# Performance work log

Hardware: AMD Instinct MI355X
Metric: run time of the kernel (lower is better)

Reference implementation:

```python
import jax, jax.numpy as jnp
import numpy as np

EMBED_DIM = 1024
NUM_HEADS = 16
HEAD_DIM = EMBED_DIM // NUM_HEADS
B, QL, KVL = 2, 2048, 2048


def setup_inputs() -> dict:
    key = jax.random.key(0)
    ks = jax.random.split(key, 16)
    std = 0.02
    inp = {
        "query": jax.random.normal(ks[0], (B, QL, EMBED_DIM), jnp.float32),
        "key": jax.random.normal(ks[1], (B, KVL, EMBED_DIM), jnp.float32),
        "value": jax.random.normal(ks[2], (B, KVL, EMBED_DIM), jnp.float32),
        "logit_scale": jax.random.uniform(ks[3], (1,), jnp.float32),
        "logit_bias": jax.random.normal(ks[4], (1,), jnp.float32),
        "Wq": jax.random.normal(ks[5], (EMBED_DIM, EMBED_DIM), jnp.float32) * std,
        "bq": jnp.zeros((EMBED_DIM,), jnp.float32),
        "Wk": jax.random.normal(ks[6], (EMBED_DIM, EMBED_DIM), jnp.float32) * std,
        "bk": jnp.zeros((EMBED_DIM,), jnp.float32),
        "Wv": jax.random.normal(ks[7], (EMBED_DIM, EMBED_DIM), jnp.float32) * std,
        "bv": jnp.zeros((EMBED_DIM,), jnp.float32),
        "Wo": jax.random.normal(ks[8], (EMBED_DIM, EMBED_DIM), jnp.float32) * std,
        "bo": jnp.zeros((EMBED_DIM,), jnp.float32),
    }
    return inp


def reference(query, key, value, logit_scale, logit_bias, Wq, bq, Wk, bk, Wv, bv, Wo, bo):
    # projections (torch Linear: x @ W.T + b)
    q = query @ Wq.T + bq    # [B, QL, D]
    k = key @ Wk.T + bk      # [B, KVL, D]
    v = value @ Wv.T + bv    # [B, KVL, D]

    # QK L2-normalization over the FULL embed_dim (before head split), per source
    q = q / jnp.linalg.norm(q, axis=-1, keepdims=True)
    k = k / jnp.linalg.norm(k, axis=-1, keepdims=True)
    scale = jnp.exp(logit_scale)  # [1], broadcasts
    bias = logit_bias             # [1], broadcasts

    # split heads: [B, H, L, Dh]
    qh = q.reshape(B, QL, NUM_HEADS, HEAD_DIM).transpose(0, 2, 1, 3)
    kh = k.reshape(B, KVL, NUM_HEADS, HEAD_DIM).transpose(0, 2, 1, 3)
    vh = v.reshape(B, KVL, NUM_HEADS, HEAD_DIM).transpose(0, 2, 1, 3)

    scores = jnp.einsum("bhqd,bhkd->bhqk", qh, kh) * scale + bias  # [B,H,QL,KVL]
    attn = jax.nn.softmax(scores.astype(jnp.float32), axis=-1).astype(qh.dtype)
    # dropout p=0.0 -> identity
    out = jnp.einsum("bhqk,bhkd->bhqd", attn, vh)  # [B,H,QL,Dh]
    out = out.transpose(0, 2, 1, 3).reshape(B, QL, EMBED_DIM)
    out = out @ Wo.T + bo
    return out, attn
```

## Files before the change

kernel.cpp:

```cpp
#include <hip/hip_runtime.h>

#define B_   2
#define L_   2048
#define D_   1024
#define H_   16
#define DH_  64
#define M_TOT (B_ * L_)

typedef __attribute__((ext_vector_type(8))) __bf16 bf16x8;
typedef __attribute__((ext_vector_type(4))) float f32x4;
typedef __attribute__((ext_vector_type(8))) unsigned short u16x8;

__device__ __forceinline__ unsigned short f2bf(float f) {
    unsigned int u = __float_as_uint(f);
    u += 0x7fffu + ((u >> 16) & 1u);
    return (unsigned short)(u >> 16);
}
__device__ __forceinline__ float bf2f(unsigned short u) {
    return __uint_as_float(((unsigned int)u) << 16);
}

__device__ __forceinline__ void gload_lds16(const void* g, void* l) {
    __builtin_amdgcn_global_load_lds(
        (__attribute__((address_space(1))) void*)(void*)g,
        (__attribute__((address_space(3))) void*)l, 16, 0, 0);
}

__global__ __launch_bounds__(256) void cast_in(const float* __restrict__ src,
                                               u16x8* __restrict__ dst)
{
    const int i = blockIdx.x * 256 + threadIdx.x;
    const float4* s = (const float4*)src;
    float4 a = s[2 * i], b = s[2 * i + 1];
    u16x8 w;
    w[0] = f2bf(a.x); w[1] = f2bf(a.y); w[2] = f2bf(a.z); w[3] = f2bf(a.w);
    w[4] = f2bf(b.x); w[5] = f2bf(b.y); w[6] = f2bf(b.z); w[7] = f2bf(b.w);
    dst[i] = w;
}

__global__ __launch_bounds__(256) void cast_w4(const float* __restrict__ Wq,
                                               const float* __restrict__ Wk,
                                               const float* __restrict__ Wv,
                                               const float* __restrict__ Wo,
                                               u16x8* __restrict__ dst)
{
    const int y = blockIdx.y;
    const float* src = (y == 0) ? Wq : (y == 1) ? Wk : (y == 2) ? Wv : Wo;
    const int i = blockIdx.x * 256 + threadIdx.x;
    const float4* s = (const float4*)src;
    float4 a = s[2 * i], b = s[2 * i + 1];
    u16x8 w;
    w[0] = f2bf(a.x); w[1] = f2bf(a.y); w[2] = f2bf(a.z); w[3] = f2bf(a.w);
    w[4] = f2bf(b.x); w[5] = f2bf(b.y); w[6] = f2bf(b.z); w[7] = f2bf(b.w);
    dst[(size_t)y * (D_ * D_ / 8) + i] = w;
}

template<bool F32OUT>
__global__ __launch_bounds__(256) void gemm_nt_mfma(
    const unsigned short* __restrict__ A, const unsigned short* __restrict__ W,
    const float* __restrict__ bias, void* __restrict__ Cout, int K, int N)
{
    __shared__ __align__(16) unsigned short As[128 * 64];
    __shared__ __align__(16) unsigned short Bs[128 * 64];
    const int tid  = threadIdx.x;
    const int bm   = blockIdx.x * 128;
    const int bn   = blockIdx.y * 128;
    const int lane = tid & 63, wid = tid >> 6;
    const int wm   = (wid >> 1) * 64, wn = (wid & 1) * 64;
    const int kg   = lane >> 4, lr = lane & 15;
    const int swz  = lr & 7;

    f32x4 zero = {0.f, 0.f, 0.f, 0.f};
    f32x4 acc[4][4];
    #pragma unroll
    for (int m = 0; m < 4; ++m)
        #pragma unroll
        for (int n = 0; n < 4; ++n) acc[m][n] = zero;

    for (int k0 = 0; k0 < K; k0 += 64) {
        __syncthreads();
        #pragma unroll
        for (int i = 0; i < 4; ++i) {
            int c   = i * 256 + tid;
            int row = c >> 3;
            int c8  = (c & 7) ^ (row & 7);
            gload_lds16(A + (size_t)(bm + row) * K + k0 + c8 * 8, (char*)As + c * 16);
            gload_lds16(W + (size_t)(bn + row) * K + k0 + c8 * 8, (char*)Bs + c * 16);
        }
        __syncthreads();
        #pragma unroll
        for (int ks = 0; ks < 2; ++ks) {
            bf16x8 af[4], bfr[4];
            #pragma unroll
            for (int m = 0; m < 4; ++m)
                af[m] = *(const bf16x8*)((const char*)As +
                        (wm + m * 16 + lr) * 128 + (((ks * 4 + kg) ^ swz) << 4));
            #pragma unroll
            for (int n = 0; n < 4; ++n)
                bfr[n] = *(const bf16x8*)((const char*)Bs +
                        (wn + n * 16 + lr) * 128 + (((ks * 4 + kg) ^ swz) << 4));
            #pragma unroll
            for (int m = 0; m < 4; ++m)
                #pragma unroll
                for (int n = 0; n < 4; ++n)
                    acc[m][n] = __builtin_amdgcn_mfma_f32_16x16x32_bf16(
                        af[m], bfr[n], acc[m][n], 0, 0, 0);
        }
    }

    #pragma unroll
    for (int n = 0; n < 4; ++n) {
        const int col = bn + wn + n * 16 + lr;
        const float bv = bias[col];
        #pragma unroll
        for (int m = 0; m < 4; ++m) {
            const int row0 = bm + wm + m * 16 + kg * 4;
            #pragma unroll
            for (int r = 0; r < 4; ++r) {
                float val = acc[m][n][r] + bv;
                if (F32OUT)
                    ((float*)Cout)[(size_t)(row0 + r) * N + col] = val;
                else
                    ((unsigned short*)Cout)[(size_t)(row0 + r) * N + col] = f2bf(val);
            }
        }
    }
}

__global__ __launch_bounds__(256) void attn_sums(
    const unsigned short* __restrict__ qn, const unsigned short* __restrict__ kn,
    const float* __restrict__ ls, const float* __restrict__ lb,
    float* __restrict__ sums)
{
    __shared__ __align__(16) unsigned short Qs[128 * 64];
    __shared__ __align__(16) unsigned short Ks[128 * 64];
    __shared__ float red[2][128];
    const int z = blockIdx.y, b = z >> 4, h = z & 15;
    const unsigned short* Qp = qn + (size_t)b * L_ * D_ + h * DH_;
    const unsigned short* Kp = kn + (size_t)b * L_ * D_ + h * DH_;

    const int tid  = threadIdx.x;
    const int bm   = blockIdx.x * 128;
    const int lane = tid & 63, wid = tid >> 6;
    const int wq   = wid >> 1, wkv = wid & 1;
    const int kg   = lane >> 4, lr = lane & 15;
    const int swz  = lr & 7;

    #pragma unroll
    for (int i = 0; i < 4; ++i) {
        int c = i * 256 + tid, row = c >> 3, c8 = (c & 7) ^ (row & 7);
        gload_lds16(Qp + (size_t)(bm + row) * D_ + c8 * 8, (char*)Qs + c * 16);
    }

    const float scale = expf(ls[0]);
    const float sb = lb[0];
    f32x4 zero = {0.f, 0.f, 0.f, 0.f};
    float rs[4][4] = {};

    for (int kv0 = 0; kv0 < L_; kv0 += 128) {
        __syncthreads();
        #pragma unroll
        for (int i = 0; i < 4; ++i) {
            int c = i * 256 + tid, row = c >> 3, c8 = (c & 7) ^ (row & 7);
            gload_lds16(Kp + (size_t)(kv0 + row) * D_ + c8 * 8, (char*)Ks + c * 16);
        }
        __syncthreads();
        f32x4 s[4][4];
        #pragma unroll
        for (int m = 0; m < 4; ++m)
            #pragma unroll
            for (int n = 0; n < 4; ++n) s[m][n] = zero;
        #pragma unroll
        for (int ks = 0; ks < 2; ++ks) {
            bf16x8 af[4], bfr[4];
            #pragma unroll
            for (int m = 0; m < 4; ++m)
                af[m] = *(const bf16x8*)((const char*)Qs +
                        (wq * 64 + m * 16 + lr) * 128 + (((ks * 4 + kg) ^ swz) << 4));
            #pragma unroll
            for (int n = 0; n < 4; ++n)
                bfr[n] = *(const bf16x8*)((const char*)Ks +
                        (wkv * 64 + n * 16 + lr) * 128 + (((ks * 4 + kg) ^ swz) << 4));
            #pragma unroll
            for (int m = 0; m < 4; ++m)
                #pragma unroll
                for (int n = 0; n < 4; ++n)
                    s[m][n] = __builtin_amdgcn_mfma_f32_16x16x32_bf16(
                        af[m], bfr[n], s[m][n], 0, 0, 0);
        }
        #pragma unroll
        for (int m = 0; m < 4; ++m)
            #pragma unroll
            for (int n = 0; n < 4; ++n)
                #pragma unroll
                for (int r = 0; r < 4; ++r)
                    rs[m][r] += __expf(s[m][n][r] * scale + sb);
    }

    #pragma unroll
    for (int m = 0; m < 4; ++m)
        #pragma unroll
        for (int r = 0; r < 4; ++r) {
            float sv = rs[m][r];
            sv += __shfl_xor(sv, 1); sv += __shfl_xor(sv, 2);
            sv += __shfl_xor(sv, 4); sv += __shfl_xor(sv, 8);
            if (lr == 0) red[wkv][wq * 64 + m * 16 + kg * 4 + r] = sv;
        }
    __syncthreads();
    if (tid < 128)
        sums[(size_t)z * L_ + bm + tid] = red[0][tid] + red[1][tid];
}

__global__ __launch_bounds__(256) void attn_fused(
    const unsigned short* __restrict__ qn, const unsigned short* __restrict__ kn,
    const unsigned short* __restrict__ Vt, const float* __restrict__ sums,
    const float* __restrict__ ls, const float* __restrict__ lb,
    float* __restrict__ attn, unsigned short* __restrict__ ctx)
{
    __shared__ __align__(16) unsigned short Qs[64 * 64];
    __shared__ __align__(16) unsigned short Ks[128 * 64];
    __shared__ __align__(16) unsigned short Vs[64 * 128];
    __shared__ __align__(16) unsigned short Ps[64 * 128];
    __shared__ float invs[64];
    const int z = blockIdx.y, b = z >> 4, h = z & 15;
    const unsigned short* Qp = qn + (size_t)b * L_ * D_ + h * DH_;
    const unsigned short* Kp = kn + (size_t)b * L_ * D_ + h * DH_;
    const unsigned short* Vp = Vt + (size_t)z * DH_ * L_;
    float* Cp = attn + (size_t)z * L_ * L_;
    unsigned short* Op = ctx + (size_t)b * L_ * D_ + h * DH_;

    const int tid  = threadIdx.x;
    const int bm   = blockIdx.x * 64;
    const int lane = tid & 63, wid = tid >> 6;
    const int wq   = wid >> 1, wkv = wid & 1;
    const int kg   = lane >> 4, lr = lane & 15;
    const int swz  = lr & 7;

    #pragma unroll
    for (int i = 0; i < 2; ++i) {
        int c = i * 256 + tid, row = c >> 3, c8 = (c & 7) ^ (row & 7);
        gload_lds16(Qp + (size_t)(bm + row) * D_ + c8 * 8, (char*)Qs + c * 16);
    }
    if (tid < 64) invs[tid] = 1.0f / sums[(size_t)z * L_ + bm + tid];

    const float scale = expf(ls[0]);
    const float sb = lb[0];
    f32x4 zero = {0.f, 0.f, 0.f, 0.f};
    f32x4 cacc[2][2];
    #pragma unroll
    for (int m = 0; m < 2; ++m) { cacc[m][0] = zero; cacc[m][1] = zero; }

    for (int kv0 = 0; kv0 < L_; kv0 += 128) {
        __syncthreads();
        #pragma unroll
        for (int i = 0; i < 4; ++i) {
            int c = i * 256 + tid, row = c >> 3, c8 = (c & 7) ^ (row & 7);
            gload_lds16(Kp + (size_t)(kv0 + row) * D_ + c8 * 8, (char*)Ks + c * 16);
        }
        #pragma unroll
        for (int i = 0; i < 4; ++i) {
            int c = i * 256 + tid, row = c >> 4, cc = c & 15;
            int sc = cc ^ (row & 7);
            gload_lds16(Vp + (size_t)row * L_ + kv0 + sc * 8, (char*)Vs + c * 16);
        }
        __syncthreads();

        f32x4 s[2][4];
        #pragma unroll
        for (int m = 0; m < 2; ++m)
            #pragma unroll
            for (int n = 0; n < 4; ++n) s[m][n] = zero;
        #pragma unroll
        for (int ks = 0; ks < 2; ++ks) {
            bf16x8 af[2], bfr[4];
            #pragma unroll
            for (int m = 0; m < 2; ++m)
                af[m] = *(const bf16x8*)((const char*)Qs +
                        (wq * 32 + m * 16 + lr) * 128 + (((ks * 4 + kg) ^ swz) << 4));
            #pragma unroll
            for (int n = 0; n < 4; ++n)
                bfr[n] = *(const bf16x8*)((const char*)Ks +
                        (wkv * 64 + n * 16 + lr) * 128 + (((ks * 4 + kg) ^ swz) << 4));
            #pragma unroll
            for (int m = 0; m < 2; ++m)
                #pragma unroll
                for (int n = 0; n < 4; ++n)
                    s[m][n] = __builtin_amdgcn_mfma_f32_16x16x32_bf16(
                        af[m], bfr[n], s[m][n], 0, 0, 0);
        }

        #pragma unroll
        for (int n = 0; n < 4; ++n) {
            #pragma unroll
            for (int m = 0; m < 2; ++m) {
                #pragma unroll
                for (int r = 0; r < 4; ++r) {
                    int row_l = wq * 32 + m * 16 + kg * 4 + r;
                    int col_l = wkv * 64 + n * 16 + lr;
                    float e = __expf(s[m][n][r] * scale + sb) * invs[row_l];
                    Cp[(size_t)(bm + row_l) * L_ + kv0 + col_l] = e;
                    int chunk = (col_l >> 3) ^ (row_l & 7);
                    Ps[row_l * 128 + chunk * 8 + (col_l & 7)] = f2bf(e);
                }
            }
        }
        __syncthreads();

        #pragma unroll
        for (int k4 = 0; k4 < 4; ++k4) {
            bf16x8 pa[2], vb[2];
            #pragma unroll
            for (int m = 0; m < 2; ++m)
                pa[m] = *(const bf16x8*)((const char*)Ps +
                        (wq * 32 + m * 16 + lr) * 256 + (((k4 * 4 + kg) ^ swz) << 4));
            #pragma unroll
            for (int n = 0; n < 2; ++n)
                vb[n] = *(const bf16x8*)((const char*)Vs +
                        (wkv * 32 + n * 16 + lr) * 256 + (((k4 * 4 + kg) ^ swz) << 4));
            #pragma unroll
            for (int m = 0; m < 2; ++m)
                #pragma unroll
                for (int n = 0; n < 2; ++n)
                    cacc[m][n] = __builtin_amdgcn_mfma_f32_16x16x32_bf16(
                        pa[m], vb[n], cacc[m][n], 0, 0, 0);
        }
    }

    #pragma unroll
    for (int n = 0; n < 2; ++n) {
        const int col = wkv * 32 + n * 16 + lr;
        #pragma unroll
        for (int m = 0; m < 2; ++m) {
            const int row0 = bm + wq * 32 + m * 16 + kg * 4;
            #pragma unroll
            for (int r = 0; r < 4; ++r)
                Op[(size_t)(row0 + r) * D_ + col] = f2bf(cacc[m][n][r]);
        }
    }
}

__global__ __launch_bounds__(256) void transpose_v(
    const unsigned short* __restrict__ v8, unsigned short* __restrict__ Vt)
{
    __shared__ unsigned short tile[64][66];
    const int z = blockIdx.y, b = z >> 4, h = z & 15;
    const int t0 = blockIdx.x * 64;
    const unsigned short* src = v8 + ((size_t)(b * L_ + t0)) * D_ + h * DH_;
    unsigned short* dst = Vt + (size_t)z * DH_ * L_ + t0;
    const int t = threadIdx.x;
    #pragma unroll
    for (int i = 0; i < 2; ++i) {
        int c = i * 256 + t;
        int r = c >> 3, c8 = c & 7;
        u16x8 v = *(const u16x8*)(src + (size_t)r * D_ + c8 * 8);
        #pragma unroll
        for (int e = 0; e < 8; ++e) tile[r][c8 * 8 + e] = v[e];
    }
    __syncthreads();
    #pragma unroll
    for (int i = 0; i < 2; ++i) {
        int c = i * 256 + t;
        int d = c >> 3, c8 = c & 7;
        u16x8 v;
        #pragma unroll
        for (int e = 0; e < 8; ++e) v[e] = tile[c8 * 8 + e][d];
        *(u16x8*)(dst + (size_t)d * L_ + c8 * 8) = v;
    }
}

__global__ __launch_bounds__(256) void l2norm_bf16(unsigned short* __restrict__ x)
{
    unsigned short* row = x + (size_t)blockIdx.x * D_;
    const int tid = threadIdx.x;
    ushort4 v = ((ushort4*)row)[tid];
    float f0 = bf2f(v.x), f1 = bf2f(v.y), f2 = bf2f(v.z), f3 = bf2f(v.w);
    float ss = f0 * f0 + f1 * f1 + f2 * f2 + f3 * f3;
    #pragma unroll
    for (int off = 32; off >= 1; off >>= 1)
        ss += __shfl_xor(ss, off);
    __shared__ float red[4];
    const int lane = tid & 63, wid = tid >> 6;
    if (lane == 0) red[wid] = ss;
    __syncthreads();
    ss = red[0] + red[1] + red[2] + red[3];
    const float inv = rsqrtf(ss);
    ushort4 o;
    o.x = f2bf(f0 * inv); o.y = f2bf(f1 * inv);
    o.z = f2bf(f2 * inv); o.w = f2bf(f3 * inv);
    ((ushort4*)row)[tid] = o;
}

extern "C" void kernel_launch(void* const* d_in, const int* in_sizes, int n_in,
                              void* d_out, int out_size, void* d_ws, size_t ws_size,
                              hipStream_t stream)
{
    const float* query = (const float*)d_in[0];
    const float* key_  = (const float*)d_in[1];
    const float* value = (const float*)d_in[2];
    const float* ls    = (const float*)d_in[3];
    const float* lb    = (const float*)d_in[4];
    const float* Wq    = (const float*)d_in[5];
    const float* bq    = (const float*)d_in[6];
    const float* Wk    = (const float*)d_in[7];
    const float* bk    = (const float*)d_in[8];
    const float* Wv    = (const float*)d_in[9];
    const float* bv    = (const float*)d_in[10];
    const float* Wo    = (const float*)d_in[11];
    const float* bo    = (const float*)d_in[12];

    float* out  = (float*)d_out;
    float* attn = out + (size_t)M_TOT * D_;

    unsigned short* xb = (unsigned short*)d_ws;
    unsigned short* Wb = xb + (size_t)M_TOT * D_;
    unsigned short* q8 = Wb + (size_t)4 * D_ * D_;
    unsigned short* k8 = q8 + (size_t)M_TOT * D_;
    unsigned short* v8 = k8 + (size_t)M_TOT * D_;
    unsigned short* Vt = v8 + (size_t)M_TOT * D_;
    unsigned short* ctxb = xb;
    float* sums = (float*)v8;

    dim3 blk(256);
    const dim3 gproj(M_TOT / 128, D_ / 128);

    cast_w4<<<dim3(D_ * D_ / 8 / 256, 4), blk, 0, stream>>>(Wq, Wk, Wv, Wo, (u16x8*)Wb);

    cast_in<<<M_TOT * D_ / 8 / 256, blk, 0, stream>>>(query, (u16x8*)xb);
    gemm_nt_mfma<false><<<gproj, blk, 0, stream>>>(xb, Wb + 0 * (size_t)D_ * D_, bq, q8, D_, D_);
    cast_in<<<M_TOT * D_ / 8 / 256, blk, 0, stream>>>(key_, (u16x8*)xb);
    gemm_nt_mfma<false><<<gproj, blk, 0, stream>>>(xb, Wb + 1 * (size_t)D_ * D_, bk, k8, D_, D_);
    cast_in<<<M_TOT * D_ / 8 / 256, blk, 0, stream>>>(value, (u16x8*)xb);
    gemm_nt_mfma<false><<<gproj, blk, 0, stream>>>(xb, Wb + 2 * (size_t)D_ * D_, bv, v8, D_, D_);

    l2norm_bf16<<<dim3(M_TOT), blk, 0, stream>>>(q8);
    l2norm_bf16<<<dim3(M_TOT), blk, 0, stream>>>(k8);

    transpose_v<<<dim3(L_ / 64, B_ * H_), blk, 0, stream>>>(v8, Vt);

    attn_sums<<<dim3(L_ / 128, B_ * H_), blk, 0, stream>>>(q8, k8, ls, lb, sums);

    attn_fused<<<dim3(L_ / 64, B_ * H_), blk, 0, stream>>>(
        q8, k8, Vt, sums, ls, lb, attn, ctxb);

    gemm_nt_mfma<true><<<gproj, blk, 0, stream>>>(ctxb, Wb + 3 * (size_t)D_ * D_, bo, out, D_, D_);
}
```

Baseline: 826.5 us.

## Double-buffer GEMM and attention tiles, shrink tiles, remap blocks, merge l2norm launches

The projection GEMM moves to a 128x64 tile with double-buffered LDS prefetch of the next K slice. attn_sums and attn_fused also double-buffer their K/V tiles and use a flat block index that interleaves heads across blocks, presumably for L2 locality. attn_fused drops to 64-wide KV tiles, splits the PV product across warps and reduces it through LDS. The two l2norm launches merge into one. Together these aim to hide global load latency and raise occupancy, at the cost of more LDS per block, an extra reduction step, and a removed barrier before the P·V reads that relies on an explicit waitcnt.

```diff
diff --git a/kernel.cpp b/kernel.cpp
--- a/kernel.cpp
+++ b/kernel.cpp
@@ -56,60 +56,78 @@
 }
 
 template<bool F32OUT>
-__global__ __launch_bounds__(256) void gemm_nt_mfma(
+__global__ __launch_bounds__(256, 3) void gemm_nt_mfma(
     const unsigned short* __restrict__ A, const unsigned short* __restrict__ W,
     const float* __restrict__ bias, void* __restrict__ Cout, int K, int N)
 {
-    __shared__ __align__(16) unsigned short As[128 * 64];
-    __shared__ __align__(16) unsigned short Bs[128 * 64];
+    __shared__ __align__(16) unsigned short As[2][128 * 64];
+    __shared__ __align__(16) unsigned short Bs[2][64 * 64];
     const int tid  = threadIdx.x;
     const int bm   = blockIdx.x * 128;
-    const int bn   = blockIdx.y * 128;
+    const int bn   = blockIdx.y * 64;
     const int lane = tid & 63, wid = tid >> 6;
-    const int wm   = (wid >> 1) * 64, wn = (wid & 1) * 64;
+    const int wm   = (wid >> 1) * 64, wn = (wid & 1) * 32;
     const int kg   = lane >> 4, lr = lane & 15;
     const int swz  = lr & 7;
 
     f32x4 zero = {0.f, 0.f, 0.f, 0.f};
-    f32x4 acc[4][4];
-    #pragma unroll
-    for (int m = 0; m < 4; ++m)
-        #pragma unroll
-        for (int n = 0; n < 4; ++n) acc[m][n] = zero;
-
-    for (int k0 = 0; k0 < K; k0 += 64) {
+    f32x4 acc[4][2];
+    #pragma unroll
+    for (int m = 0; m < 4; ++m) { acc[m][0] = zero; acc[m][1] = zero; }
+
+    #pragma unroll
+    for (int i = 0; i < 4; ++i) {
+        int c = i * 256 + tid, row = c >> 3, c8 = (c & 7) ^ (row & 7);
+        gload_lds16(A + (size_t)(bm + row) * K + c8 * 8, (char*)As[0] + c * 16);
+    }
+    #pragma unroll
+    for (int i = 0; i < 2; ++i) {
+        int c = i * 256 + tid, row = c >> 3, c8 = (c & 7) ^ (row & 7);
+        gload_lds16(W + (size_t)(bn + row) * K + c8 * 8, (char*)Bs[0] + c * 16);
+    }
+
+    const int nIt = K / 64;
+    int cur = 0;
+    for (int it = 0; it < nIt; ++it) {
         __syncthreads();
-        #pragma unroll
-        for (int i = 0; i < 4; ++i) {
-            int c   = i * 256 + tid;
-            int row = c >> 3;
-            int c8  = (c & 7) ^ (row & 7);
-            gload_lds16(A + (size_t)(bm + row) * K + k0 + c8 * 8, (char*)As + c * 16);
-            gload_lds16(W + (size_t)(bn + row) * K + k0 + c8 * 8, (char*)Bs + c * 16);
-        }
-        __syncthreads();
+        if (it + 1 < nIt) {
+            const int k0 = (it + 1) * 64;
+            #pragma unroll
+            for (int i = 0; i < 4; ++i) {
+                int c = i * 256 + tid, row = c >> 3, c8 = (c & 7) ^ (row & 7);
+                gload_lds16(A + (size_t)(bm + row) * K + k0 + c8 * 8,
+                            (char*)As[cur ^ 1] + c * 16);
+            }
+            #pragma unroll
+            for (int i = 0; i < 2; ++i) {
+                int c = i * 256 + tid, row = c >> 3, c8 = (c & 7) ^ (row & 7);
+                gload_lds16(W + (size_t)(bn + row) * K + k0 + c8 * 8,
+                            (char*)Bs[cur ^ 1] + c * 16);
+            }
+        }
         #pragma unroll
         for (int ks = 0; ks < 2; ++ks) {
-            bf16x8 af[4], bfr[4];
+            bf16x8 af[4], bfr[2];
             #pragma unroll
             for (int m = 0; m < 4; ++m)
-                af[m] = *(const bf16x8*)((const char*)As +
+                af[m] = *(const bf16x8*)((const char*)As[cur] +
                         (wm + m * 16 + lr) * 128 + (((ks * 4 + kg) ^ swz) << 4));
             #pragma unroll
-            for (int n = 0; n < 4; ++n)
-                bfr[n] = *(const bf16x8*)((const char*)Bs +
+            for (int n = 0; n < 2; ++n)
+                bfr[n] = *(const bf16x8*)((const char*)Bs[cur] +
                         (wn + n * 16 + lr) * 128 + (((ks * 4 + kg) ^ swz) << 4));
             #pragma unroll
             for (int m = 0; m < 4; ++m)
                 #pragma unroll
-                for (int n = 0; n < 4; ++n)
+                for (int n = 0; n < 2; ++n)
                     acc[m][n] = __builtin_amdgcn_mfma_f32_16x16x32_bf16(
                         af[m], bfr[n], acc[m][n], 0, 0, 0);
         }
-    }
-
-    #pragma unroll
-    for (int n = 0; n < 4; ++n) {
+        cur ^= 1;
+    }
+
+    #pragma unroll
+    for (int n = 0; n < 2; ++n) {
         const int col = bn + wn + n * 16 + lr;
         const float bv = bias[col];
         #pragma unroll
@@ -127,44 +145,56 @@
     }
 }
 
-__global__ __launch_bounds__(256) void attn_sums(
+__global__ __launch_bounds__(256, 3) void attn_sums(
     const unsigned short* __restrict__ qn, const unsigned short* __restrict__ kn,
     const float* __restrict__ ls, const float* __restrict__ lb,
     float* __restrict__ sums)
 {
     __shared__ __align__(16) unsigned short Qs[128 * 64];
-    __shared__ __align__(16) unsigned short Ks[128 * 64];
+    __shared__ __align__(16) unsigned short Ks[2][128 * 64];
     __shared__ float red[2][128];
-    const int z = blockIdx.y, b = z >> 4, h = z & 15;
+    const int flat = blockIdx.x;
+    const int z  = (flat & 7) * 4 + ((flat >> 3) & 3);
+    const int qt = flat >> 5;
+    const int b = z >> 4, h = z & 15;
     const unsigned short* Qp = qn + (size_t)b * L_ * D_ + h * DH_;
     const unsigned short* Kp = kn + (size_t)b * L_ * D_ + h * DH_;
 
-    const int tid  = threadIdx.x;
-    const int bm   = blockIdx.x * 128;
+    const int tid = threadIdx.x;
+    const int bm  = qt * 128;
     const int lane = tid & 63, wid = tid >> 6;
-    const int wq   = wid >> 1, wkv = wid & 1;
-    const int kg   = lane >> 4, lr = lane & 15;
-    const int swz  = lr & 7;
+    const int wq = wid >> 1, wkv = wid & 1;
+    const int kg = lane >> 4, lr = lane & 15;
+    const int swz = lr & 7;
 
     #pragma unroll
     for (int i = 0; i < 4; ++i) {
         int c = i * 256 + tid, row = c >> 3, c8 = (c & 7) ^ (row & 7);
         gload_lds16(Qp + (size_t)(bm + row) * D_ + c8 * 8, (char*)Qs + c * 16);
+    }
+    #pragma unroll
+    for (int i = 0; i < 4; ++i) {
+        int c = i * 256 + tid, row = c >> 3, c8 = (c & 7) ^ (row & 7);
+        gload_lds16(Kp + (size_t)row * D_ + c8 * 8, (char*)Ks[0] + c * 16);
     }
 
     const float scale = expf(ls[0]);
     const float sb = lb[0];
     f32x4 zero = {0.f, 0.f, 0.f, 0.f};
     float rs[4][4] = {};
-
-    for (int kv0 = 0; kv0 < L_; kv0 += 128) {
+    int cur = 0;
+
+    for (int it = 0; it < L_ / 128; ++it) {
         __syncthreads();
-        #pragma unroll
-        for (int i = 0; i < 4; ++i) {
-            int c = i * 256 + tid, row = c >> 3, c8 = (c & 7) ^ (row & 7);
-            gload_lds16(Kp + (size_t)(kv0 + row) * D_ + c8 * 8, (char*)Ks + c * 16);
-        }
-        __syncthreads();
+        if (it + 1 < L_ / 128) {
+            const int kv = (it + 1) * 128;
+            #pragma unroll
+            for (int i = 0; i < 4; ++i) {
+                int c = i * 256 + tid, row = c >> 3, c8 = (c & 7) ^ (row & 7);
+                gload_lds16(Kp + (size_t)(kv + row) * D_ + c8 * 8,
+                            (char*)Ks[cur ^ 1] + c * 16);
+            }
+        }
         f32x4 s[4][4];
         #pragma unroll
         for (int m = 0; m < 4; ++m)
@@ -179,7 +209,7 @@
                         (wq * 64 + m * 16 + lr) * 128 + (((ks * 4 + kg) ^ swz) << 4));
             #pragma unroll
             for (int n = 0; n < 4; ++n)
-                bfr[n] = *(const bf16x8*)((const char*)Ks +
+                bfr[n] = *(const bf16x8*)((const char*)Ks[cur] +
                         (wkv * 64 + n * 16 + lr) * 128 + (((ks * 4 + kg) ^ swz) << 4));
             #pragma unroll
             for (int m = 0; m < 4; ++m)
@@ -195,6 +225,7 @@
                 #pragma unroll
                 for (int r = 0; r < 4; ++r)
                     rs[m][r] += __expf(s[m][n][r] * scale + sb);
+        cur ^= 1;
     }
 
     #pragma unroll
@@ -211,130 +242,166 @@
         sums[(size_t)z * L_ + bm + tid] = red[0][tid] + red[1][tid];
 }
 
-__global__ __launch_bounds__(256) void attn_fused(
+__global__ __launch_bounds__(256, 3) void attn_fused(
     const unsigned short* __restrict__ qn, const unsigned short* __restrict__ kn,
     const unsigned short* __restrict__ Vt, const float* __restrict__ sums,
     const float* __restrict__ ls, const float* __restrict__ lb,
     float* __restrict__ attn, unsigned short* __restrict__ ctx)
 {
     __shared__ __align__(16) unsigned short Qs[64 * 64];
-    __shared__ __align__(16) unsigned short Ks[128 * 64];
-    __shared__ __align__(16) unsigned short Vs[64 * 128];
-    __shared__ __align__(16) unsigned short Ps[64 * 128];
+    __shared__ __align__(16) unsigned short Ks[2][64 * 64];
+    __shared__ __align__(16) unsigned short Vs[2][64 * 64];
+    __shared__ __align__(16) unsigned short Ps[64 * 64];
     __shared__ float invs[64];
-    const int z = blockIdx.y, b = z >> 4, h = z & 15;
+    const int flat = blockIdx.x;
+    const int z  = (flat & 7) * 4 + ((flat >> 3) & 3);
+    const int qt = flat >> 5;
+    const int b = z >> 4, h = z & 15;
     const unsigned short* Qp = qn + (size_t)b * L_ * D_ + h * DH_;
     const unsigned short* Kp = kn + (size_t)b * L_ * D_ + h * DH_;
     const unsigned short* Vp = Vt + (size_t)z * DH_ * L_;
     float* Cp = attn + (size_t)z * L_ * L_;
     unsigned short* Op = ctx + (size_t)b * L_ * D_ + h * DH_;
 
-    const int tid  = threadIdx.x;
-    const int bm   = blockIdx.x * 64;
+    const int tid = threadIdx.x;
+    const int bm  = qt * 64;
     const int lane = tid & 63, wid = tid >> 6;
-    const int wq   = wid >> 1, wkv = wid & 1;
-    const int kg   = lane >> 4, lr = lane & 15;
-    const int swz  = lr & 7;
+    const int wq = wid >> 1, wkv = wid & 1;
+    const int kg = lane >> 4, lr = lane & 15;
+    const int swz = lr & 7;
 
     #pragma unroll
     for (int i = 0; i < 2; ++i) {
         int c = i * 256 + tid, row = c >> 3, c8 = (c & 7) ^ (row & 7);
         gload_lds16(Qp + (size_t)(bm + row) * D_ + c8 * 8, (char*)Qs + c * 16);
+    }
+    #pragma unroll
+    for (int i = 0; i < 2; ++i) {
+        int c = i * 256 + tid, row = c >> 3, c8 = (c & 7) ^ (row & 7);
+        gload_lds16(Kp + (size_t)row * D_ + c8 * 8, (char*)Ks[0] + c * 16);
+    }
+    #pragma unroll
+    for (int i = 0; i < 2; ++i) {
+        int c = i * 256 + tid, row = c >> 3, c8 = (c & 7) ^ (row & 7);
+        gload_lds16(Vp + (size_t)row * L_ + c8 * 8, (char*)Vs[0] + c * 16);
     }
     if (tid < 64) invs[tid] = 1.0f / sums[(size_t)z * L_ + bm + tid];
 
     const float scale = expf(ls[0]);
     const float sb = lb[0];
     f32x4 zero = {0.f, 0.f, 0.f, 0.f};
-    f32x4 cacc[2][2];
-    #pragma unroll
-    for (int m = 0; m < 2; ++m) { cacc[m][0] = zero; cacc[m][1] = zero; }
-
-    for (int kv0 = 0; kv0 < L_; kv0 += 128) {
+    f32x4 cacc[2][4];
+    #pragma unroll
+    for (int m = 0; m < 2; ++m)
+        #pragma unroll
+        for (int n = 0; n < 4; ++n) cacc[m][n] = zero;
+
+    int cur = 0;
+    for (int it = 0; it < L_ / 64; ++it) {
         __syncthreads();
-        #pragma unroll
-        for (int i = 0; i < 4; ++i) {
-            int c = i * 256 + tid, row = c >> 3, c8 = (c & 7) ^ (row & 7);
-            gload_lds16(Kp + (size_t)(kv0 + row) * D_ + c8 * 8, (char*)Ks + c * 16);
-        }
-        #pragma unroll
-        for (int i = 0; i < 4; ++i) {
-            int c = i * 256 + tid, row = c >> 4, cc = c & 15;
-            int sc = cc ^ (row & 7);
-            gload_lds16(Vp + (size_t)row * L_ + kv0 + sc * 8, (char*)Vs + c * 16);
-        }
-        __syncthreads();
-
-        f32x4 s[2][4];
-        #pragma unroll
-        for (int m = 0; m < 2; ++m)
-            #pragma unroll
-            for (int n = 0; n < 4; ++n) s[m][n] = zero;
+        if (it + 1 < L_ / 64) {
+            const int kv = (it + 1) * 64;
+            #pragma unroll
+            for (int i = 0; i < 2; ++i) {
+                int c = i * 256 + tid, row = c >> 3, c8 = (c & 7) ^ (row & 7);
+                gload_lds16(Kp + (size_t)(kv + row) * D_ + c8 * 8,
+                            (char*)Ks[cur ^ 1] + c * 16);
+            }
+            #pragma unroll
+            for (int i = 0; i < 2; ++i) {
+                int c = i * 256 + tid, row = c >> 3, c8 = (c & 7) ^ (row & 7);
+                gload_lds16(Vp + (size_t)row * L_ + kv + c8 * 8,
+                            (char*)Vs[cur ^ 1] + c * 16);
+            }
+        }
+
+        f32x4 s[2][2];
+        #pragma unroll
+        for (int m = 0; m < 2; ++m) { s[m][0] = zero; s[m][1] = zero; }
         #pragma unroll
         for (int ks = 0; ks < 2; ++ks) {
-            bf16x8 af[2], bfr[4];
+            bf16x8 af[2], bfr[2];
             #pragma unroll
             for (int m = 0; m < 2; ++m)
                 af[m] = *(const bf16x8*)((const char*)Qs +
                         (wq * 32 + m * 16 + lr) * 128 + (((ks * 4 + kg) ^ swz) << 4));
             #pragma unroll
-            for (int n = 0; n < 4; ++n)
-                bfr[n] = *(const bf16x8*)((const char*)Ks +
-                        (wkv * 64 + n * 16 + lr) * 128 + (((ks * 4 + kg) ^ swz) << 4));
+            for (int n = 0; n < 2; ++n)
+                bfr[n] = *(const bf16x8*)((const char*)Ks[cur] +
+                        (wkv * 32 + n * 16 + lr) * 128 + (((ks * 4 + kg) ^ swz) << 4));
             #pragma unroll
             for (int m = 0; m < 2; ++m)
                 #pragma unroll
-                for (int n = 0; n < 4; ++n)
+                for (int n = 0; n < 2; ++n)
                     s[m][n] = __builtin_amdgcn_mfma_f32_16x16x32_bf16(
                         af[m], bfr[n], s[m][n], 0, 0, 0);
         }
 
-        #pragma unroll
-        for (int n = 0; n < 4; ++n) {
-            #pragma unroll
-            for (int m = 0; m < 2; ++m) {
+        const int kv0 = it * 64;
+        #pragma unroll
+        for (int m = 0; m < 2; ++m) {
+            #pragma unroll
+            for (int n = 0; n < 2; ++n) {
                 #pragma unroll
                 for (int r = 0; r < 4; ++r) {
-                    int row_l = wq * 32 + m * 16 + kg * 4 + r;
-                    int col_l = wkv * 64 + n * 16 + lr;
+                    const int row_l = wq * 32 + m * 16 + kg * 4 + r;
+                    const int col_l = wkv * 32 + n * 16 + lr;
                     float e = __expf(s[m][n][r] * scale + sb) * invs[row_l];
                     Cp[(size_t)(bm + row_l) * L_ + kv0 + col_l] = e;
-                    int chunk = (col_l >> 3) ^ (row_l & 7);
-                    Ps[row_l * 128 + chunk * 8 + (col_l & 7)] = f2bf(e);
+                    Ps[row_l * 64 + (((col_l >> 3) ^ (row_l & 7)) << 3) + (col_l & 7)]
+                        = f2bf(e);
                 }
             }
         }
-        __syncthreads();
-
-        #pragma unroll
-        for (int k4 = 0; k4 < 4; ++k4) {
-            bf16x8 pa[2], vb[2];
+        asm volatile("s_waitcnt lgkmcnt(0)" ::: "memory");
+        __builtin_amdgcn_sched_barrier(0);
+
+        {
+            bf16x8 pa[2], vb[4];
             #pragma unroll
             for (int m = 0; m < 2; ++m)
                 pa[m] = *(const bf16x8*)((const char*)Ps +
-                        (wq * 32 + m * 16 + lr) * 256 + (((k4 * 4 + kg) ^ swz) << 4));
-            #pragma unroll
-            for (int n = 0; n < 2; ++n)
-                vb[n] = *(const bf16x8*)((const char*)Vs +
-                        (wkv * 32 + n * 16 + lr) * 256 + (((k4 * 4 + kg) ^ swz) << 4));
+                        (wq * 32 + m * 16 + lr) * 128 + (((wkv * 4 + kg) ^ swz) << 4));
+            #pragma unroll
+            for (int n = 0; n < 4; ++n)
+                vb[n] = *(const bf16x8*)((const char*)Vs[cur] +
+                        (n * 16 + lr) * 128 + (((wkv * 4 + kg) ^ swz) << 4));
             #pragma unroll
             for (int m = 0; m < 2; ++m)
                 #pragma unroll
-                for (int n = 0; n < 2; ++n)
+                for (int n = 0; n < 4; ++n)
                     cacc[m][n] = __builtin_amdgcn_mfma_f32_16x16x32_bf16(
                         pa[m], vb[n], cacc[m][n], 0, 0, 0);
         }
-    }
-
-    #pragma unroll
-    for (int n = 0; n < 2; ++n) {
-        const int col = wkv * 32 + n * 16 + lr;
+        cur ^= 1;
+    }
+
+    __syncthreads();
+    float* redp = (float*)Ks;
+    if (wkv == 1) {
+        #pragma unroll
+        for (int m = 0; m < 2; ++m)
+            #pragma unroll
+            for (int n = 0; n < 4; ++n)
+                #pragma unroll
+                for (int r = 0; r < 4; ++r)
+                    redp[(wq * 32 + m * 16 + kg * 4 + r) * 64 + n * 16 + lr]
+                        = cacc[m][n][r];
+    }
+    __syncthreads();
+    if (wkv == 0) {
         #pragma unroll
         for (int m = 0; m < 2; ++m) {
-            const int row0 = bm + wq * 32 + m * 16 + kg * 4;
-            #pragma unroll
-            for (int r = 0; r < 4; ++r)
-                Op[(size_t)(row0 + r) * D_ + col] = f2bf(cacc[m][n][r]);
+            #pragma unroll
+            for (int n = 0; n < 4; ++n) {
+                #pragma unroll
+                for (int r = 0; r < 4; ++r) {
+                    const int row_l = wq * 32 + m * 16 + kg * 4 + r;
+                    const int col   = n * 16 + lr;
+                    float val = cacc[m][n][r] + redp[row_l * 64 + col];
+                    Op[(size_t)(bm + row_l) * D_ + col] = f2bf(val);
+                }
+            }
         }
     }
 }
@@ -368,9 +435,11 @@
     }
 }
 
-__global__ __launch_bounds__(256) void l2norm_bf16(unsigned short* __restrict__ x)
-{
-    unsigned short* row = x + (size_t)blockIdx.x * D_;
+__global__ __launch_bounds__(256) void l2norm2(unsigned short* __restrict__ q8,
+                                               unsigned short* __restrict__ k8)
+{
+    unsigned short* base = blockIdx.y ? k8 : q8;
+    unsigned short* row = base + (size_t)blockIdx.x * D_;
     const int tid = threadIdx.x;
     ushort4 v = ((ushort4*)row)[tid];
     float f0 = bf2f(v.x), f1 = bf2f(v.y), f2 = bf2f(v.z), f3 = bf2f(v.w);
@@ -421,7 +490,7 @@
     float* sums = (float*)v8;
 
     dim3 blk(256);
-    const dim3 gproj(M_TOT / 128, D_ / 128);
+    const dim3 gproj(M_TOT / 128, D_ / 64);
 
     cast_w4<<<dim3(D_ * D_ / 8 / 256, 4), blk, 0, stream>>>(Wq, Wk, Wv, Wo, (u16x8*)Wb);
 
@@ -432,15 +501,13 @@
     cast_in<<<M_TOT * D_ / 8 / 256, blk, 0, stream>>>(value, (u16x8*)xb);
     gemm_nt_mfma<false><<<gproj, blk, 0, stream>>>(xb, Wb + 2 * (size_t)D_ * D_, bv, v8, D_, D_);
 
-    l2norm_bf16<<<dim3(M_TOT), blk, 0, stream>>>(q8);
-    l2norm_bf16<<<dim3(M_TOT), blk, 0, stream>>>(k8);
+    l2norm2<<<dim3(M_TOT, 2), blk, 0, stream>>>(q8, k8);
 
     transpose_v<<<dim3(L_ / 64, B_ * H_), blk, 0, stream>>>(v8, Vt);
 
-    attn_sums<<<dim3(L_ / 128, B_ * H_), blk, 0, stream>>>(q8, k8, ls, lb, sums);
-
-    attn_fused<<<dim3(L_ / 64, B_ * H_), blk, 0, stream>>>(
-        q8, k8, Vt, sums, ls, lb, attn, ctxb);
+    attn_sums<<<dim3(512), blk, 0, stream>>>(q8, k8, ls, lb, sums);
+
+    attn_fused<<<dim3(1024), blk, 0, stream>>>(q8, k8, Vt, sums, ls, lb, attn, ctxb);
 
     gemm_nt_mfma<true><<<gproj, blk, 0, stream>>>(ctxb, Wb + 3 * (size_t)D_ * D_, bo, out, D_, D_);
 }
```

Measured after the change: 801.2 us. 3.1% less time.
